# Kernel tuning notes

Hardware: AMD Instinct MI355X
Metric: run time of the kernel (lower is better)

The kernel has to match this reference:

```python
import jax, jax.numpy as jnp
import numpy as np

C_M, C_Z, C_H, H = 64, 128, 32, 8
INF = 1000000.0

def _layernorm(x, w, b, eps=1e-5):
    mu = jnp.mean(x, axis=-1, keepdims=True)
    var = jnp.var(x, axis=-1, keepdims=True)
    return (x - mu) * jax.lax.rsqrt(var + eps) * w + b

def setup_inputs() -> dict:
    key = jax.random.key(0)
    ks = jax.random.split(key, 8)
    B, S, N = 1, 256, 512
    m = jax.random.normal(ks[0], (B, S, N, C_M), dtype=jnp.float32)
    z = jax.random.normal(ks[1], (B, N, N, C_Z), dtype=jnp.float32)
    mask = jnp.ones((B, N, N), dtype=jnp.float32)
    sc = lambda f: 1.0 / np.sqrt(f)
    return {
        "m": m, "z": z, "mask": mask,
        "ln_m_w": jnp.ones((C_M,), jnp.float32), "ln_m_b": jnp.zeros((C_M,), jnp.float32),
        "ln_z_w": jnp.ones((C_Z,), jnp.float32), "ln_z_b": jnp.zeros((C_Z,), jnp.float32),
        "W_m": jax.random.normal(ks[2], (H * C_H, C_M), jnp.float32) * sc(C_M),
        "W_g": jax.random.normal(ks[3], (H * C_H, C_M), jnp.float32) * sc(C_M),
        "W_z": jax.random.normal(ks[4], (H, C_Z), jnp.float32) * sc(C_Z),
        "W_o": jax.random.normal(ks[5], (C_M, H * C_H), jnp.float32) * sc(H * C_H),
    }

def reference(m, z, mask, ln_m_w, ln_m_b, ln_z_w, ln_z_b, W_m, W_g, W_z, W_o):
    B, S, N, _ = m.shape
    m_n = _layernorm(m, ln_m_w, ln_m_b)          # (B,S,N,c_m)
    z_n = _layernorm(z, ln_z_w, ln_z_b)          # (B,N,N,c_z)
    Wm = W_m.reshape(H, C_H, C_M)
    Wg = W_g.reshape(H, C_H, C_M)
    # values per head: (B,H,S,N,c_h)
    v = jnp.einsum("bsnc,hec->bhsne", m_n, Wm)
    # pair bias logits: (B,H,N,N)
    b = jnp.einsum("bijc,hc->bhij", z_n, W_z)
    b = b + (1.0 - mask[:, None]) * (-INF)
    w = jax.nn.softmax(b, axis=-1)               # (B,H,N,N)
    # gate: (B,S,N,H*c_h)
    g = jax.nn.sigmoid(jnp.einsum("bsnc,hec->bsnhe", m_n, Wg)).reshape(B, S, N, H * C_H)
    # weighted average broadcast over S: (B,H,S,N,c_h)
    o = jnp.einsum("bhij,bhsje->bhsie", w, v)
    o = jnp.transpose(o, (0, 2, 3, 1, 4)).reshape(B, S, N, H * C_H)
    return (g * o) @ W_o.T                       # (B,S,N,c_m)
```

## Files before the change

kernel.cpp:

```cpp
#include <hip/hip_runtime.h>

#define HC 256

typedef _Float16 f16x8 __attribute__((ext_vector_type(8)));
typedef float f32x4 __attribute__((ext_vector_type(4)));

union h4u { ushort4 u; _Float16 h[4]; };
union h8u { uint4 u; f16x8 h; };

__device__ __forceinline__ float wave_sum(float v) {
    #pragma unroll
    for (int off = 32; off; off >>= 1) v += __shfl_xor(v, off);
    return v;
}
__device__ __forceinline__ float wave_max(float v) {
    #pragma unroll
    for (int off = 32; off; off >>= 1) v = fmaxf(v, __shfl_xor(v, off));
    return v;
}

__global__ __launch_bounds__(256) void k_vg(
    const float* __restrict__ m, const float* __restrict__ lw,
    const float* __restrict__ lb, const float* __restrict__ Wm,
    const float* __restrict__ Wg, _Float16* __restrict__ vt,
    _Float16* __restrict__ g)
{
    __shared__ __align__(16) _Float16 lds[2 * 128 * 72];
    _Float16* Al = lds;
    _Float16* Bl = lds + 128 * 72;

    int tid  = threadIdx.x;
    int lane = tid & 63;
    int r0 = blockIdx.x * 128;
    bool gate = (blockIdx.y >= 2);
    int c0 = (blockIdx.y & 1) * 128;
    const float* Wp = gate ? Wg : Wm;

    int srow = tid >> 1, skoff = (tid & 1) * 32;
    {
        const float4* mg = (const float4*)(m + (size_t)(r0 + srow) * 64 + skoff);
        float xv[32];
        float s1 = 0.f, s2 = 0.f;
        #pragma unroll
        for (int q = 0; q < 8; q++) {
            float4 f = mg[q];
            xv[q*4+0] = f.x; xv[q*4+1] = f.y; xv[q*4+2] = f.z; xv[q*4+3] = f.w;
            s1 += f.x + f.y + f.z + f.w;
            s2 += f.x*f.x + f.y*f.y + f.z*f.z + f.w*f.w;
        }
        s1 += __shfl_xor(s1, 1);
        s2 += __shfl_xor(s2, 1);
        float mu  = s1 * (1.0f / 64.0f);
        float var = s2 * (1.0f / 64.0f) - mu * mu;
        float inv = rsqrtf(var + 1e-5f);

        const float4* wg4 = (const float4*)(Wp + (size_t)(c0 + srow) * 64 + skoff);
        #pragma unroll
        for (int q8 = 0; q8 < 4; q8++) {
            float4 w0 = wg4[q8*2], w1 = wg4[q8*2+1];
            float wf[8] = {w0.x,w0.y,w0.z,w0.w,w1.x,w1.y,w1.z,w1.w};
            f16x8 pa, pb;
            #pragma unroll
            for (int t = 0; t < 8; t++) {
                int c = skoff + q8*8 + t;
                pa[t] = (_Float16)((xv[q8*8+t] - mu) * inv * lw[c] + lb[c]);
                pb[t] = (_Float16)wf[t];
            }
            *(f16x8*)&Al[srow * 72 + skoff + q8*8] = pa;
            *(f16x8*)&Bl[srow * 72 + skoff + q8*8] = pb;
        }
    }
    __syncthreads();

    int wv = tid >> 6;
    int mrow0 = (wv & 1) * 64, ncol0 = (wv >> 1) * 64;
    int quad = lane >> 4, lc = lane & 15;
    const _Float16* afsrc = gate ? Bl : Al;
    const _Float16* bfsrc = gate ? Al : Bl;

    f32x4 acc[4][4];
    #pragma unroll
    for (int mt = 0; mt < 4; mt++)
        #pragma unroll
        for (int nt = 0; nt < 4; nt++) { f32x4 z4 = {0.f,0.f,0.f,0.f}; acc[mt][nt] = z4; }

    #pragma unroll
    for (int kk = 0; kk < 2; kk++) {
        f16x8 af[4], bf[4];
        int kf = kk * 32 + quad * 8;
        #pragma unroll
        for (int mt = 0; mt < 4; mt++)
            af[mt] = *(const f16x8*)&afsrc[(mrow0 + mt * 16 + lc) * 72 + kf];
        #pragma unroll
        for (int nt = 0; nt < 4; nt++)
            bf[nt] = *(const f16x8*)&bfsrc[(ncol0 + nt * 16 + lc) * 72 + kf];
        #pragma unroll
        for (int mt = 0; mt < 4; mt++)
            #pragma unroll
            for (int nt = 0; nt < 4; nt++)
                acc[mt][nt] = __builtin_amdgcn_mfma_f32_16x16x32_f16(af[mt], bf[nt], acc[mt][nt], 0, 0, 0);
    }

    __syncthreads();
    #pragma unroll
    for (int mt = 0; mt < 4; mt++) {
        int yd = mrow0 + mt * 16 + quad * 4;
        #pragma unroll
        for (int nt = 0; nt < 4; nt++) {
            int xd = ncol0 + nt * 16 + lc;
            h4u pk;
            #pragma unroll
            for (int t = 0; t < 4; t++) {
                float v = acc[mt][nt][t];
                if (gate) v = 1.0f / (1.0f + __expf(-v));
                pk.h[t] = (_Float16)v;
            }
            *(ushort4*)&lds[xd * 136 + yd] = pk.u;
        }
    }
    __syncthreads();

    int s_idx = blockIdx.x >> 2;
    int j0 = (blockIdx.x & 3) * 128;
    #pragma unroll
    for (int p = 0; p < 8; p++) {
        int id = p * 256 + tid;
        int xrow = id >> 4;
        int ch = id & 15;
        uint4 val = *(const uint4*)&lds[xrow * 136 + ch * 8];
        if (!gate) {
            int cg = c0 + xrow; int hh = cg >> 5, e = cg & 31;
            *(uint4*)&vt[((size_t)hh * 8192 + s_idx * 32 + e) * 512 + j0 + ch * 8] = val;
        } else {
            *(uint4*)&g[(size_t)(r0 + xrow) * 256 + c0 + ch * 8] = val;
        }
    }
}

__global__ __launch_bounds__(256) void k_bias_softmax(
    const float* __restrict__ z, const float* __restrict__ mask,
    const float* __restrict__ lzw, const float* __restrict__ lzb,
    const float* __restrict__ Wz, _Float16* __restrict__ wout)
{
    __shared__ float WW[8][128];
    __shared__ float LG[8][512];
    __shared__ float Bh[8], Ch[8];
    __shared__ float red[4];
    int tid = threadIdx.x;
    int lane = tid & 63, wv = tid >> 6;

    for (int idx = tid; idx < 1024; idx += 256) {
        int h = idx >> 7, c = idx & 127;
        WW[h][c] = Wz[h * 128 + c] * lzw[c];
    }
    __syncthreads();
    if (tid < 8) {
        float bh = 0.f, ch = 0.f;
        for (int c = 0; c < 128; c++) {
            bh += lzb[c] * Wz[tid * 128 + c];
            ch += WW[tid][c];
        }
        Bh[tid] = bh; Ch[tid] = ch;
    }
    __syncthreads();

    int i = blockIdx.x;
    int sub = tid & 7;
    int jrow = tid >> 3;
    for (int rr = 0; rr < 16; rr++) {
        int j = rr * 32 + jrow;
        const float4* zp = (const float4*)(z + ((size_t)i * 512 + j) * 128 + sub * 16);
        float s1 = 0.f, s2 = 0.f;
        float a[8] = {0.f,0.f,0.f,0.f,0.f,0.f,0.f,0.f};
        #pragma unroll
        for (int q = 0; q < 4; q++) {
            float4 f = zp[q];
            float xs[4] = {f.x, f.y, f.z, f.w};
            #pragma unroll
            for (int t = 0; t < 4; t++) {
                float x = xs[t];
                s1 += x; s2 += x * x;
                #pragma unroll
                for (int h = 0; h < 8; h++) a[h] += x * WW[h][sub * 16 + q * 4 + t];
            }
        }
        #pragma unroll
        for (int off = 1; off < 8; off <<= 1) {
            s1 += __shfl_xor(s1, off);
            s2 += __shfl_xor(s2, off);
            #pragma unroll
            for (int h = 0; h < 8; h++) a[h] += __shfl_xor(a[h], off);
        }
        if (sub == 0) {
            float mu  = s1 * (1.0f / 128.0f);
            float var = s2 * (1.0f / 128.0f) - mu * mu;
            float inv = rsqrtf(var + 1e-5f);
            float mv  = mask[(size_t)i * 512 + j];
            float madd = (1.0f - mv) * (-1000000.0f);
            #pragma unroll
            for (int h = 0; h < 8; h++)
                LG[h][j] = inv * (a[h] - mu * Ch[h]) + Bh[h] + madd;
        }
    }
    __syncthreads();

    for (int h = 0; h < 8; h++) {
        float l0 = LG[h][tid], l1 = LG[h][tid + 256];
        float mx = wave_max(fmaxf(l0, l1));
        if (lane == 0) red[wv] = mx;
        __syncthreads();
        mx = fmaxf(fmaxf(red[0], red[1]), fmaxf(red[2], red[3]));
        __syncthreads();
        float e0 = __expf(l0 - mx), e1 = __expf(l1 - mx);
        float sm = wave_sum(e0 + e1);
        if (lane == 0) red[wv] = sm;
        __syncthreads();
        sm = red[0] + red[1] + red[2] + red[3];
        __syncthreads();
        float rs = 1.0f / sm;
        size_t base = ((size_t)h * 512 + i) * 512;
        wout[base + tid]       = (_Float16)(e0 * rs);
        wout[base + tid + 256] = (_Float16)(e1 * rs);
    }
}

__global__ __launch_bounds__(256) void k_pav(
    const _Float16* __restrict__ wgt, const _Float16* __restrict__ vt,
    _Float16* __restrict__ g)
{
    __shared__ __align__(16) _Float16 lds[2 * 128 * 72];
    _Float16* Al = lds;
    _Float16* Bl = lds + 128 * 72;
    int h = blockIdx.z;
    int i0 = blockIdx.y * 128;
    int c0 = blockIdx.x * 128;
    const _Float16* A = wgt + (size_t)h * 512 * 512;
    const _Float16* B = vt  + (size_t)h * 8192 * 512;
    int tid = threadIdx.x;
    int lane = tid & 63, wv = tid >> 6;
    int mrow0 = (wv & 1) * 64, ncol0 = (wv >> 1) * 64;
    int quad = lane >> 4, lc = lane & 15;

    f32x4 acc[4][4];
    #pragma unroll
    for (int mt = 0; mt < 4; mt++)
        #pragma unroll
        for (int nt = 0; nt < 4; nt++) { f32x4 z4 = {0.f,0.f,0.f,0.f}; acc[mt][nt] = z4; }

    int srow = tid >> 1, skoff = (tid & 1) * 32;

    for (int kb = 0; kb < 512; kb += 64) {
        const uint4* ag = (const uint4*)(A + (size_t)(i0 + srow) * 512 + kb + skoff);
        const uint4* bg = (const uint4*)(B + (size_t)(c0 + srow) * 512 + kb + skoff);
        uint4 a0 = ag[0], a1 = ag[1], a2 = ag[2], a3 = ag[3];
        uint4 b0 = bg[0], b1 = bg[1], b2 = bg[2], b3 = bg[3];
        __syncthreads();
        uint4* al = (uint4*)&Al[srow * 72 + skoff];
        uint4* bl = (uint4*)&Bl[srow * 72 + skoff];
        al[0] = a0; al[1] = a1; al[2] = a2; al[3] = a3;
        bl[0] = b0; bl[1] = b1; bl[2] = b2; bl[3] = b3;
        __syncthreads();
        #pragma unroll
        for (int kk = 0; kk < 2; kk++) {
            f16x8 af[4], bf[4];
            int kf = kk * 32 + quad * 8;
            #pragma unroll
            for (int mt = 0; mt < 4; mt++)
                af[mt] = *(const f16x8*)&Bl[(mrow0 + mt * 16 + lc) * 72 + kf];
            #pragma unroll
            for (int nt = 0; nt < 4; nt++)
                bf[nt] = *(const f16x8*)&Al[(ncol0 + nt * 16 + lc) * 72 + kf];
            #pragma unroll
            for (int mt = 0; mt < 4; mt++)
                #pragma unroll
                for (int nt = 0; nt < 4; nt++)
                    acc[mt][nt] = __builtin_amdgcn_mfma_f32_16x16x32_f16(af[mt], bf[nt], acc[mt][nt], 0, 0, 0);
        }
    }

    __syncthreads();
    #pragma unroll
    for (int mt = 0; mt < 4; mt++) {
        int yd = mrow0 + mt * 16 + quad * 4;
        #pragma unroll
        for (int nt = 0; nt < 4; nt++) {
            int xd = ncol0 + nt * 16 + lc;
            h4u pk;
            #pragma unroll
            for (int t = 0; t < 4; t++) pk.h[t] = (_Float16)acc[mt][nt][t];
            *(ushort4*)&lds[xd * 136 + yd] = pk.u;
        }
    }
    __syncthreads();

    #pragma unroll
    for (int p = 0; p < 8; p++) {
        int id = p * 256 + tid;
        int il = id >> 4;
        int ch = id & 15;
        int ng = c0 + ch * 8;
        int sj = ng >> 5, e = ng & 31;
        size_t base = ((size_t)sj * 512 + i0 + il) * HC + h * 32 + e;
        h8u ov, gv, res;
        ov.u = *(const uint4*)&lds[il * 136 + ch * 8];
        gv.u = *(const uint4*)&g[base];
        #pragma unroll
        for (int t = 0; t < 8; t++) res.h[t] = (_Float16)((float)ov.h[t] * (float)gv.h[t]);
        *(uint4*)&g[base] = res.u;
    }
}

__global__ __launch_bounds__(256) void k_out(
    const _Float16* __restrict__ og, const float* __restrict__ Wo,
    float* __restrict__ out)
{
    __shared__ __align__(16) char smem[34816];
    _Float16* Blds = (_Float16*)smem;
    float* Tf = (float*)smem;
    int tid = threadIdx.x;
    int lane = tid & 63, wv = tid >> 6;
    int r0 = blockIdx.x * 128;

    {
        const float4* src = (const float4*)(Wo + (size_t)(tid >> 2) * 256 + (tid & 3) * 64);
        #pragma unroll
        for (int q8 = 0; q8 < 8; q8++) {
            float4 w0 = src[q8*2], w1 = src[q8*2+1];
            float wf[8] = {w0.x,w0.y,w0.z,w0.w,w1.x,w1.y,w1.z,w1.w};
            f16x8 p;
            #pragma unroll
            for (int t = 0; t < 8; t++) p[t] = (_Float16)wf[t];
            *(f16x8*)&Blds[(tid >> 2) * 264 + (tid & 3) * 64 + q8 * 8] = p;
        }
    }
    __syncthreads();

    int quad = lane >> 4, lc = lane & 15;
    f32x4 acc[4][2];
    #pragma unroll
    for (int ct = 0; ct < 4; ct++)
        #pragma unroll
        for (int rt = 0; rt < 2; rt++) { f32x4 z4 = {0.f,0.f,0.f,0.f}; acc[ct][rt] = z4; }

    for (int kb = 0; kb < 256; kb += 32) {
        int kf = kb + quad * 8;
        f16x8 bf[2];
        #pragma unroll
        for (int rt = 0; rt < 2; rt++) {
            int row = r0 + wv * 32 + rt * 16 + lc;
            bf[rt] = *(const f16x8*)(og + (size_t)row * HC + kf);
        }
        f16x8 af[4];
        #pragma unroll
        for (int ct = 0; ct < 4; ct++)
            af[ct] = *(const f16x8*)&Blds[(ct * 16 + lc) * 264 + kf];
        #pragma unroll
        for (int ct = 0; ct < 4; ct++)
            #pragma unroll
            for (int rt = 0; rt < 2; rt++)
                acc[ct][rt] = __builtin_amdgcn_mfma_f32_16x16x32_f16(af[ct], bf[rt], acc[ct][rt], 0, 0, 0);
    }

    __syncthreads();
    #pragma unroll
    for (int ct = 0; ct < 4; ct++) {
        int cd = ct * 16 + quad * 4;
        #pragma unroll
        for (int rt = 0; rt < 2; rt++) {
            int rd = wv * 32 + rt * 16 + lc;
            *(f32x4*)&Tf[rd * 68 + cd] = acc[ct][rt];
        }
    }
    __syncthreads();

    #pragma unroll
    for (int p = 0; p < 8; p++) {
        int id = p * 256 + tid;
        int rl = id >> 4;
        int ch = id & 15;
        uint4 v = *(const uint4*)&Tf[rl * 68 + ch * 4];
        *(uint4*)&out[(size_t)(r0 + rl) * 64 + ch * 4] = v;
    }
}

extern "C" void kernel_launch(void* const* d_in, const int* in_sizes, int n_in,
                              void* d_out, int out_size, void* d_ws, size_t ws_size,
                              hipStream_t stream) {
    const float* m    = (const float*)d_in[0];
    const float* z    = (const float*)d_in[1];
    const float* mask = (const float*)d_in[2];
    const float* lnmw = (const float*)d_in[3];
    const float* lnmb = (const float*)d_in[4];
    const float* lnzw = (const float*)d_in[5];
    const float* lnzb = (const float*)d_in[6];
    const float* Wm   = (const float*)d_in[7];
    const float* Wg   = (const float*)d_in[8];
    const float* Wz   = (const float*)d_in[9];
    const float* Wo   = (const float*)d_in[10];
    float* out = (float*)d_out;

    char* ws = (char*)d_ws;
    _Float16* vt = (_Float16*)ws;
    _Float16* g  = (_Float16*)(ws + 67108864);
    _Float16* w  = (_Float16*)d_out;
    (void)in_sizes; (void)n_in; (void)out_size; (void)ws_size;

    k_vg<<<dim3(1024, 4), 256, 0, stream>>>(m, lnmw, lnmb, Wm, Wg, vt, g);
    k_bias_softmax<<<512, 256, 0, stream>>>(z, mask, lnzw, lnzb, Wz, w);
    k_pav<<<dim3(64, 4, 8), 256, 0, stream>>>(w, vt, g);
    k_out<<<1024, 256, 0, stream>>>(g, Wo, out);
}
```

Before: 403.3 us.

## Use direct global-to-LDS async loads with XOR swizzle in PAV GEMM; per-wave softmax

The PAV GEMM now stages its A and B tiles with global_load_lds (direct global-to-LDS 16-byte copies) instead of loading through registers and storing to LDS. It uses an XOR-swizzled unpadded layout to avoid bank conflicts, which also shrinks the LDS footprint. The bias-softmax kernel now gives each wave two whole heads and reduces them with wave shuffles only, removing the block-wide barriers and the shared reduction array. One risk: there is no explicit wait on the async loads before the barrier, so correctness depends on the compiler inserting a vmcnt wait.

```diff
diff --git a/kernel.cpp b/kernel.cpp
--- a/kernel.cpp
+++ b/kernel.cpp
@@ -17,6 +17,12 @@
     #pragma unroll
     for (int off = 32; off; off >>= 1) v = fmaxf(v, __shfl_xor(v, off));
     return v;
+}
+
+__device__ __forceinline__ void async16(_Float16* l, const _Float16* gp) {
+    __builtin_amdgcn_global_load_lds(
+        (const __attribute__((address_space(1))) void*)gp,
+        (__attribute__((address_space(3))) void*)l, 16, 0, 0);
 }
 
 __global__ __launch_bounds__(256) void k_vg(
@@ -145,7 +151,6 @@
     __shared__ float WW[8][128];
     __shared__ float LG[8][512];
     __shared__ float Bh[8], Ch[8];
-    __shared__ float red[4];
     int tid = threadIdx.x;
     int lane = tid & 63, wv = tid >> 6;
 
@@ -204,23 +209,29 @@
     }
     __syncthreads();
 
-    for (int h = 0; h < 8; h++) {
-        float l0 = LG[h][tid], l1 = LG[h][tid + 256];
-        float mx = wave_max(fmaxf(l0, l1));
-        if (lane == 0) red[wv] = mx;
-        __syncthreads();
-        mx = fmaxf(fmaxf(red[0], red[1]), fmaxf(red[2], red[3]));
-        __syncthreads();
-        float e0 = __expf(l0 - mx), e1 = __expf(l1 - mx);
-        float sm = wave_sum(e0 + e1);
-        if (lane == 0) red[wv] = sm;
-        __syncthreads();
-        sm = red[0] + red[1] + red[2] + red[3];
-        __syncthreads();
-        float rs = 1.0f / sm;
+    #pragma unroll
+    for (int hh = 0; hh < 2; hh++) {
+        int h = wv * 2 + hh;
+        float l[8];
+        float mx = -1e30f;
+        #pragma unroll
+        for (int q = 0; q < 8; q++) {
+            l[q] = LG[h][lane + q * 64];
+            mx = fmaxf(mx, l[q]);
+        }
+        mx = wave_max(mx);
+        float s = 0.f;
+        #pragma unroll
+        for (int q = 0; q < 8; q++) {
+            l[q] = __expf(l[q] - mx);
+            s += l[q];
+        }
+        s = wave_sum(s);
+        float rs = 1.0f / s;
         size_t base = ((size_t)h * 512 + i) * 512;
-        wout[base + tid]       = (_Float16)(e0 * rs);
-        wout[base + tid + 256] = (_Float16)(e1 * rs);
+        #pragma unroll
+        for (int q = 0; q < 8; q++)
+            wout[base + lane + q * 64] = (_Float16)(l[q] * rs);
     }
 }
 
@@ -228,9 +239,9 @@
     const _Float16* __restrict__ wgt, const _Float16* __restrict__ vt,
     _Float16* __restrict__ g)
 {
-    __shared__ __align__(16) _Float16 lds[2 * 128 * 72];
+    __shared__ __align__(16) _Float16 lds[128 * 136];
     _Float16* Al = lds;
-    _Float16* Bl = lds + 128 * 72;
+    _Float16* Bl = lds + 128 * 64;
     int h = blockIdx.z;
     int i0 = blockIdx.y * 128;
     int c0 = blockIdx.x * 128;
@@ -241,44 +252,46 @@
     int mrow0 = (wv & 1) * 64, ncol0 = (wv >> 1) * 64;
     int quad = lane >> 4, lc = lane & 15;
 
+    int rsub = lane >> 3;
+    int csw  = ((lane & 7) ^ rsub) * 8;
+
     f32x4 acc[4][4];
     #pragma unroll
     for (int mt = 0; mt < 4; mt++)
         #pragma unroll
         for (int nt = 0; nt < 4; nt++) { f32x4 z4 = {0.f,0.f,0.f,0.f}; acc[mt][nt] = z4; }
 
-    int srow = tid >> 1, skoff = (tid & 1) * 32;
-
     for (int kb = 0; kb < 512; kb += 64) {
-        const uint4* ag = (const uint4*)(A + (size_t)(i0 + srow) * 512 + kb + skoff);
-        const uint4* bg = (const uint4*)(B + (size_t)(c0 + srow) * 512 + kb + skoff);
-        uint4 a0 = ag[0], a1 = ag[1], a2 = ag[2], a3 = ag[3];
-        uint4 b0 = bg[0], b1 = bg[1], b2 = bg[2], b3 = bg[3];
+        #pragma unroll
+        for (int t = 0; t < 4; t++) {
+            int r = wv * 32 + t * 8;
+            async16(&Al[r * 64], A + (size_t)(i0 + r + rsub) * 512 + kb + csw);
+            async16(&Bl[r * 64], B + (size_t)(c0 + r + rsub) * 512 + kb + csw);
+        }
         __syncthreads();
-        uint4* al = (uint4*)&Al[srow * 72 + skoff];
-        uint4* bl = (uint4*)&Bl[srow * 72 + skoff];
-        al[0] = a0; al[1] = a1; al[2] = a2; al[3] = a3;
-        bl[0] = b0; bl[1] = b1; bl[2] = b2; bl[3] = b3;
-        __syncthreads();
+
         #pragma unroll
         for (int kk = 0; kk < 2; kk++) {
             f16x8 af[4], bf[4];
-            int kf = kk * 32 + quad * 8;
-            #pragma unroll
-            for (int mt = 0; mt < 4; mt++)
-                af[mt] = *(const f16x8*)&Bl[(mrow0 + mt * 16 + lc) * 72 + kf];
-            #pragma unroll
-            for (int nt = 0; nt < 4; nt++)
-                bf[nt] = *(const f16x8*)&Al[(ncol0 + nt * 16 + lc) * 72 + kf];
+            #pragma unroll
+            for (int mt = 0; mt < 4; mt++) {
+                int r = mrow0 + mt * 16 + lc;
+                af[mt] = *(const f16x8*)&Bl[r * 64 + (((kk * 4 + quad) ^ (r & 7)) << 3)];
+            }
+            #pragma unroll
+            for (int nt = 0; nt < 4; nt++) {
+                int r = ncol0 + nt * 16 + lc;
+                bf[nt] = *(const f16x8*)&Al[r * 64 + (((kk * 4 + quad) ^ (r & 7)) << 3)];
+            }
             #pragma unroll
             for (int mt = 0; mt < 4; mt++)
                 #pragma unroll
                 for (int nt = 0; nt < 4; nt++)
                     acc[mt][nt] = __builtin_amdgcn_mfma_f32_16x16x32_f16(af[mt], bf[nt], acc[mt][nt], 0, 0, 0);
         }
-    }
-
-    __syncthreads();
+        __syncthreads();
+    }
+
     #pragma unroll
     for (int mt = 0; mt < 4; mt++) {
         int yd = mrow0 + mt * 16 + quad * 4;
```

After: 399.7 us. About the same (-0.9%).
